# Kernel tuning notes

Hardware: AMD Instinct MI355X
Metric: run time of the kernel (lower is better)

The kernel has to match this reference:

```python
import jax, jax.numpy as jnp
import numpy as np

N_NODES = 50000
NEG_SLOPE = 0.2


def _gat_conv(x, edge_index, W, att_src, att_dst, bias, heads, out_ch, concat):
    """PyG-style GATConv (add_self_loops=True, negative_slope=0.2).
    x: [N, F_in], edge_index: [2, E] (row=src, row=dst), W: [F_in, heads*out_ch],
    att_src/att_dst: [heads, out_ch], bias: [heads*out_ch] or [out_ch]."""
    N = x.shape[0]
    # add self-loops
    loops = jnp.arange(N, dtype=edge_index.dtype)
    src = jnp.concatenate([edge_index[0], loops])
    dst = jnp.concatenate([edge_index[1], loops])

    h = (x @ W).reshape(N, heads, out_ch)                 # [N, H, C]
    a_src = jnp.einsum('nhc,hc->nh', h, att_src)          # [N, H]
    a_dst = jnp.einsum('nhc,hc->nh', h, att_dst)          # [N, H]

    e = a_src[src] + a_dst[dst]                           # [E', H]
    e = jnp.where(e >= 0, e, NEG_SLOPE * e)               # leaky_relu

    # segment softmax over incoming edges of each dst node
    e_max = jax.ops.segment_max(e, dst, num_segments=N)   # [N, H]
    e_max = jnp.where(jnp.isfinite(e_max), e_max, 0.0)
    ex = jnp.exp(e - e_max[dst])                          # [E', H]
    denom = jax.ops.segment_sum(ex, dst, num_segments=N)  # [N, H]
    alpha = ex / (denom[dst] + 1e-16)                     # [E', H]

    msg = alpha[:, :, None] * h[src]                      # [E', H, C]
    out = jax.ops.segment_sum(msg, dst, num_segments=N)   # [N, H, C]

    if concat:
        out = out.reshape(N, heads * out_ch)
    else:
        out = out.mean(axis=1)
    return out + bias


def setup_inputs() -> dict:
    key = jax.random.key(0)
    ks = jax.random.split(key, 12)
    F_in, hid, H1, C, H2 = 512, 8, 8, 40, 1
    x = jax.random.normal(ks[0], (N_NODES, F_in), dtype=jnp.float32)
    edge_index = jax.random.randint(ks[1], (2, 1600000), 0, N_NODES, dtype=jnp.int64)
    s1 = 1.0 / np.sqrt(F_in)
    s2 = 1.0 / np.sqrt(hid * H1)
    return {
        'x': x,
        'edge_index': edge_index,
        'W1': jax.random.normal(ks[2], (F_in, H1 * hid), dtype=jnp.float32) * s1,
        'att_src1': jax.random.normal(ks[3], (H1, hid), dtype=jnp.float32) * s2,
        'att_dst1': jax.random.normal(ks[4], (H1, hid), dtype=jnp.float32) * s2,
        'b1': jnp.zeros((H1 * hid,), dtype=jnp.float32),
        'W2': jax.random.normal(ks[5], (H1 * hid, H2 * C), dtype=jnp.float32) * s2,
        'att_src2': jax.random.normal(ks[6], (H2, C), dtype=jnp.float32) * 0.15,
        'att_dst2': jax.random.normal(ks[7], (H2, C), dtype=jnp.float32) * 0.15,
        'b2': jnp.zeros((C,), dtype=jnp.float32),
    }


def reference(x, edge_index, W1, att_src1, att_dst1, b1, W2, att_src2, att_dst2, b2):
    # eval mode: dropout is identity
    h = _gat_conv(x, edge_index, W1, att_src1, att_dst1, b1, heads=8, out_ch=8, concat=True)
    h = jax.nn.relu(h)
    h = _gat_conv(h, edge_index, W2, att_src2, att_dst2, b2, heads=1, out_ch=40, concat=False)
    return jax.nn.log_softmax(h, axis=1)
```

## Files before the change

kernel.cpp:

```cpp
#include <hip/hip_runtime.h>
#include <math.h>

#define NNODES 50000
#define NEG_SLOPE 0.2f
#define NB 391
#define BW 128
#define CHUNK 4096
#define CAP 8128

typedef __bf16 bf16x8 __attribute__((ext_vector_type(8)));
typedef float f32x4 __attribute__((ext_vector_type(4)));

__device__ inline float rlane(float v, int l) {
    return __uint_as_float(__builtin_amdgcn_readlane((int)__float_as_uint(v), l));
}

__global__ void prep(const float* __restrict__ W1, __bf16* __restrict__ W1b,
                     int* __restrict__ bcur) {
    int i = blockIdx.x * 256 + threadIdx.x;
    if (i < NB) bcur[i] = i * CAP;
    else if (i == NB) bcur[NB] = 0;
    if (i >= 512 * 64) return;
    int k = i >> 6, n = i & 63;
    W1b[((size_t)(k >> 3) * 64 + n) * 8 + (k & 7)] = (__bf16)W1[i];
}

__global__ __launch_bounds__(256) void bin_scatter(const int* __restrict__ ei,
                                                   int E, int N, int* bcur,
                                                   int* __restrict__ tmp) {
    __shared__ int lcnt[NB];
    __shared__ int lbase[NB];
    int tid = threadIdx.x;
    int base0 = blockIdx.x * CHUNK;
    int lim = min(base0 + CHUNK, E + N);
    for (int i = tid; i < NB; i += 256) lcnt[i] = 0;
    __syncthreads();
    for (int e = base0 + tid; e < lim; e += 256) {
        int d = (e < E) ? ei[E + e] : e - E;
        atomicAdd(&lcnt[d >> 7], 1);
    }
    __syncthreads();
    for (int b = tid; b < NB; b += 256) {
        int c = lcnt[b];
        lbase[b] = c ? atomicAdd(&bcur[b], c) : 0;
    }
    __syncthreads();
    for (int i = tid; i < NB; i += 256) lcnt[i] = 0;
    __syncthreads();
    for (int e = base0 + tid; e < lim; e += 256) {
        int s, d;
        if (e < E) { s = ei[e]; d = ei[E + e]; }
        else       { s = d = e - E; }
        int b = d >> 7;
        int p = atomicAdd(&lcnt[b], 1);
        tmp[lbase[b] + p] = ((d & 127) << 16) | s;
    }
}

__global__ __launch_bounds__(256) void csr_finalize(int* __restrict__ bcur,
                                                    const int* __restrict__ tmp,
                                                    int N, int* __restrict__ off,
                                                    int* __restrict__ off_end,
                                                    int* __restrict__ slot) {
    __shared__ int cnt[BW];
    __shared__ int cur[BW];
    __shared__ int cbase_s;
    int b = blockIdx.x, tid = threadIdx.x;
    int base = b * CAP;
    int m = bcur[b] - base;
    if (tid < BW) cnt[tid] = 0;
    __syncthreads();
    for (int i = tid; i < m; i += 256)
        atomicAdd(&cnt[(tmp[base + i] >> 16) & 127], 1);
    __syncthreads();
    if (tid == 0) cbase_s = atomicAdd(&bcur[NB], m);
    int myv = (tid < BW) ? cnt[tid] : 0;
    for (int o = 1; o < BW; o <<= 1) {
        int u = 0;
        if (tid >= o && tid < BW) u = cnt[tid - o];
        __syncthreads();
        if (tid < BW) cnt[tid] += u;
        __syncthreads();
    }
    if (tid < BW) {
        int ex = cbase_s + cnt[tid] - myv;
        cur[tid] = ex;
        int g = b * BW + tid;
        if (g < N) { off[g] = ex; off_end[g] = ex + myv; }
    }
    __syncthreads();
    for (int i = tid; i < m; i += 256) {
        int v = tmp[base + i];
        int k = (v >> 16) & 127;
        int p = atomicAdd(&cur[k], 1);
        slot[p] = v & 0xFFFF;
    }
}

__global__ __launch_bounds__(256) void gemm1_mfma(const float* __restrict__ X,
                                                  const __bf16* __restrict__ W1b,
                                                  const float* __restrict__ att_s1,
                                                  const float* __restrict__ att_d1,
                                                  __bf16* __restrict__ H1b,
                                                  float* __restrict__ a_s1,
                                                  float* __restrict__ a_d1,
                                                  int M) {
    __shared__ __bf16 As[2048];
    __shared__ __bf16 Bs[2048];
    int tid = threadIdx.x, wid = tid >> 6, lane = tid & 63;
    int quad = lane >> 4, l15 = lane & 15;
    int m0 = blockIdx.x * 64;
    f32x4 acc[4] = {{0.f, 0.f, 0.f, 0.f}, {0.f, 0.f, 0.f, 0.f},
                    {0.f, 0.f, 0.f, 0.f}, {0.f, 0.f, 0.f, 0.f}};
    int mrow = tid >> 2;
    int kq_w = tid & 3;
    int xrow = min(m0 + mrow, M - 1);
    const float* xp = X + (size_t)xrow * 512 + kq_w * 8;
    for (int kb = 0; kb < 16; ++kb) {
        float4 xa = *(const float4*)(xp + kb * 32);
        float4 xb = *(const float4*)(xp + kb * 32 + 4);
        bf16x8 av;
        av[0] = (__bf16)xa.x; av[1] = (__bf16)xa.y;
        av[2] = (__bf16)xa.z; av[3] = (__bf16)xa.w;
        av[4] = (__bf16)xb.x; av[5] = (__bf16)xb.y;
        av[6] = (__bf16)xb.z; av[7] = (__bf16)xb.w;
        *(bf16x8*)(As + ((size_t)kq_w * 64 + mrow) * 8) = av;
        *(bf16x8*)(Bs + ((size_t)wid * 64 + lane) * 8) =
            *(const bf16x8*)(W1b + ((size_t)(kb * 4 + wid) * 64 + lane) * 8);
        __syncthreads();
        bf16x8 af = *(const bf16x8*)(As + ((size_t)quad * 64 + 16 * wid + l15) * 8);
#pragma unroll
        for (int t = 0; t < 4; ++t) {
            bf16x8 bf = *(const bf16x8*)(Bs + ((size_t)quad * 64 + 16 * t + l15) * 8);
            acc[t] = __builtin_amdgcn_mfma_f32_16x16x32_bf16(af, bf, acc[t], 0, 0, 0);
        }
        __syncthreads();
    }
    float asv[4], adv[4];
#pragma unroll
    for (int t = 0; t < 4; ++t) {
        asv[t] = att_s1[16 * t + l15];
        adv[t] = att_d1[16 * t + l15];
    }
#pragma unroll
    for (int t = 0; t < 4; ++t) {
#pragma unroll
        for (int r = 0; r < 4; ++r) {
            int gm = m0 + 16 * wid + quad * 4 + r;
            if (gm < M) H1b[(size_t)gm * 64 + 16 * t + l15] = (__bf16)acc[t][r];
            float ps = acc[t][r] * asv[t];
            float pd = acc[t][r] * adv[t];
            ps += __shfl_xor(ps, 1); ps += __shfl_xor(ps, 2); ps += __shfl_xor(ps, 4);
            pd += __shfl_xor(pd, 1); pd += __shfl_xor(pd, 2); pd += __shfl_xor(pd, 4);
            if (gm < M && (l15 & 7) == 0) {
                int hh = 2 * t + (l15 >> 3);
                a_s1[(size_t)gm * 8 + hh] = ps;
                a_d1[(size_t)gm * 8 + hh] = pd;
            }
        }
    }
}

#define EDGE_GROUP1(IDX, SVAR, WVAR, HVAR, EVAR)                        \
    int SVAR = __shfl(sv, ((IDX) < deg) ? (IDX) : dm1);                 \
    float EVAR = a_src[(size_t)SVAR * 8 + eh] + adst_c;                 \
    EVAR = (EVAR >= 0.f) ? EVAR : NEG_SLOPE * EVAR;                     \
    float WVAR = ((IDX) < deg) ? __expf(EVAR) : 0.f;                    \
    bf16x8 HVAR = *(const bf16x8*)(hbase + (size_t)SVAR * 64);

__global__ __launch_bounds__(256, 8) void agg1_fused(const int* __restrict__ off,
                                                  const int* __restrict__ off_end,
                                                  const int* __restrict__ slot,
                                                  const __bf16* __restrict__ H1b,
                                                  const float* __restrict__ a_src,
                                                  const float* __restrict__ a_dst,
                                                  const float* __restrict__ b1,
                                                  const float* __restrict__ W2,
                                                  const float* __restrict__ att_src2,
                                                  const float* __restrict__ att_dst2,
                                                  __bf16* __restrict__ H2b,
                                                  float* __restrict__ a_s2,
                                                  float* __restrict__ a_d2) {
    __shared__ float W2s[64 * 40];
    int tid = threadIdx.x;
    int wid = tid >> 6, lane = tid & 63;
    for (int i = tid; i < 64 * 40; i += 256) W2s[i] = W2[i];
    int d = blockIdx.x * 4 + wid;
    int beg = off[d], end = off_end[d];
    int deg = end - beg, dm1 = deg - 1;
    int es = lane >> 3;
    int eh = lane & 7;
    float adst_c = a_dst[(size_t)d * 8 + eh];
    const __bf16* hbase = H1b + eh * 8;
    int sv = slot[beg + ((lane < deg) ? lane : dm1)];
    float acc[8] = {0.f, 0.f, 0.f, 0.f, 0.f, 0.f, 0.f, 0.f};
    float den_l = 0.f;
    {
        EDGE_GROUP1(es,      s0, w0, h0, e0)
        EDGE_GROUP1(8 + es,  s1, w1, h1, e1)
        EDGE_GROUP1(16 + es, s2, w2, h2, e2)
        EDGE_GROUP1(24 + es, s3, w3, h3, e3)
        den_l = ((w0 + w1) + (w2 + w3));
#pragma unroll
        for (int q = 0; q < 8; ++q)
            acc[q] = w0 * (float)h0[q] + w1 * (float)h1[q] +
                     w2 * (float)h2[q] + w3 * (float)h3[q];
    }
    int dcap = (deg < 64) ? deg : 64;
    for (int b = 32; b < dcap; b += 16) {
        EDGE_GROUP1(b + es,     s0, w0, h0, e0)
        EDGE_GROUP1(b + 8 + es, s1, w1, h1, e1)
        den_l += w0 + w1;
#pragma unroll
        for (int q = 0; q < 8; ++q)
            acc[q] += w0 * (float)h0[q] + w1 * (float)h1[q];
    }
    for (int i = beg + 64; i < end; i += 8) {
        int j = i + es;
        int jj = (j < end) ? j : (end - 1);
        int s = slot[jj];
        float e = a_src[(size_t)s * 8 + eh] + adst_c;
        e = (e >= 0.f) ? e : NEG_SLOPE * e;
        float w = (j < end) ? __expf(e) : 0.f;
        den_l += w;
        bf16x8 hv = *(const bf16x8*)(hbase + (size_t)s * 64);
#pragma unroll
        for (int q = 0; q < 8; ++q) acc[q] += w * (float)hv[q];
    }
#pragma unroll
    for (int m = 8; m <= 32; m <<= 1) {
        den_l += __shfl_xor(den_l, m);
#pragma unroll
        for (int q = 0; q < 8; ++q) acc[q] += __shfl_xor(acc[q], m);
    }
    float rden = 1.f / (den_l + 1e-16f);
    float vr[8];
#pragma unroll
    for (int q = 0; q < 8; ++q) {
        float t = acc[q] * rden + b1[eh * 8 + q];
        vr[q] = (t > 0.f) ? t : 0.f;
    }
    __syncthreads();
    int c = lane, cc = (c < 40) ? c : 0;
    float acc2a = 0.f, acc2b = 0.f;
#pragma unroll
    for (int k = 0; k < 64; k += 2) {
        float r0 = rlane(vr[k & 7], k >> 3);
        float r1 = rlane(vr[(k + 1) & 7], (k + 1) >> 3);
        acc2a += r0 * W2s[k * 40 + cc];
        acc2b += r1 * W2s[(k + 1) * 40 + cc];
    }
    float acc2 = acc2a + acc2b;
    H2b[(size_t)d * 64 + c] = (__bf16)((c < 40) ? acc2 : 0.f);
    float ps = (c < 40) ? acc2 * att_src2[cc] : 0.f;
    float pd = (c < 40) ? acc2 * att_dst2[cc] : 0.f;
#pragma unroll
    for (int mm = 32; mm >= 1; mm >>= 1) {
        ps += __shfl_xor(ps, mm);
        pd += __shfl_xor(pd, mm);
    }
    if (lane == 0) { a_s2[d] = ps; a_d2[d] = pd; }
}

#define EDGE_GROUP2(IDX, SVAR, WVAR, HVAR, EVAR)                        \
    int SVAR = __shfl(sv, ((IDX) < deg) ? (IDX) : dm1);                 \
    float EVAR = a_src2[SVAR] + adst;                                   \
    EVAR = (EVAR >= 0.f) ? EVAR : NEG_SLOPE * EVAR;                     \
    float WVAR = ((IDX) < deg) ? __expf(EVAR) : 0.f;                    \
    bf16x8 HVAR = *(const bf16x8*)(hbase + (size_t)SVAR * 64);

__global__ __launch_bounds__(256, 8) void agg2(const int* __restrict__ off,
                                            const int* __restrict__ off_end,
                                            const int* __restrict__ slot,
                                            const __bf16* __restrict__ H2b,
                                            const float* __restrict__ a_src2,
                                            const float* __restrict__ a_d2,
                                            const float* __restrict__ b2,
                                            float* __restrict__ out) {
    int tid = threadIdx.x;
    int wid = tid >> 6, lane = tid & 63;
    int d = blockIdx.x * 4 + wid;
    int beg = off[d], end = off_end[d];
    int deg = end - beg, dm1 = deg - 1;
    int es = lane >> 3;
    int sl = lane & 7;
    float adst = a_d2[d];
    const __bf16* hbase = H2b + sl * 8;
    bool valid = (sl < 5);
    int sv = slot[beg + ((lane < deg) ? lane : dm1)];
    float acc[8] = {0.f, 0.f, 0.f, 0.f, 0.f, 0.f, 0.f, 0.f};
    float den_l = 0.f;
    {
        EDGE_GROUP2(es,      s0, w0, h0, e0)
        EDGE_GROUP2(8 + es,  s1, w1, h1, e1)
        EDGE_GROUP2(16 + es, s2, w2, h2, e2)
        EDGE_GROUP2(24 + es, s3, w3, h3, e3)
        den_l = ((w0 + w1) + (w2 + w3));
#pragma unroll
        for (int q = 0; q < 8; ++q)
            acc[q] = w0 * (float)h0[q] + w1 * (float)h1[q] +
                     w2 * (float)h2[q] + w3 * (float)h3[q];
    }
    int dcap = (deg < 64) ? deg : 64;
    for (int b = 32; b < dcap; b += 16) {
        EDGE_GROUP2(b + es,     s0, w0, h0, e0)
        EDGE_GROUP2(b + 8 + es, s1, w1, h1, e1)
        den_l += w0 + w1;
#pragma unroll
        for (int q = 0; q < 8; ++q)
            acc[q] += w0 * (float)h0[q] + w1 * (float)h1[q];
    }
    for (int i = beg + 64; i < end; i += 8) {
        int j = i + es;
        int jj = (j < end) ? j : (end - 1);
        int s = slot[jj];
        float e = a_src2[s] + adst;
        e = (e >= 0.f) ? e : NEG_SLOPE * e;
        float w = (j < end) ? __expf(e) : 0.f;
        den_l += w;
        bf16x8 hv = *(const bf16x8*)(hbase + (size_t)s * 64);
#pragma unroll
        for (int q = 0; q < 8; ++q) acc[q] += w * (float)hv[q];
    }
#pragma unroll
    for (int m = 8; m <= 32; m <<= 1) {
        den_l += __shfl_xor(den_l, m);
#pragma unroll
        for (int q = 0; q < 8; ++q) acc[q] += __shfl_xor(acc[q], m);
    }
    float rden = 1.f / (den_l + 1e-16f);
    float v[8];
    float vm = -3.0e38f;
#pragma unroll
    for (int q = 0; q < 8; ++q) {
        v[q] = acc[q] * rden + b2[valid ? sl * 8 + q : 0];
        vm = fmaxf(vm, v[q]);
    }
    if (!valid) vm = -3.0e38f;
#pragma unroll
    for (int m = 1; m <= 4; m <<= 1) vm = fmaxf(vm, __shfl_xor(vm, m));
    float se = 0.f;
#pragma unroll
    for (int q = 0; q < 8; ++q) se += __expf(v[q] - vm);
    if (!valid) se = 0.f;
#pragma unroll
    for (int m = 1; m <= 4; m <<= 1) se += __shfl_xor(se, m);
    float lse = vm + __logf(se);
    if (es == 0 && valid) {
        f32x4 o0 = {v[0] - lse, v[1] - lse, v[2] - lse, v[3] - lse};
        f32x4 o1 = {v[4] - lse, v[5] - lse, v[6] - lse, v[7] - lse};
        *(f32x4*)(out + (size_t)d * 40 + sl * 8) = o0;
        *(f32x4*)(out + (size_t)d * 40 + sl * 8 + 4) = o1;
    }
}

extern "C" void kernel_launch(void* const* d_in, const int* in_sizes, int n_in,
                              void* d_out, int out_size, void* d_ws, size_t ws_size,
                              hipStream_t stream) {
    const float* x   = (const float*)d_in[0];
    const int*   ei  = (const int*)d_in[1];
    const float* W1  = (const float*)d_in[2];
    const float* as1 = (const float*)d_in[3];
    const float* ad1 = (const float*)d_in[4];
    const float* b1  = (const float*)d_in[5];
    const float* W2  = (const float*)d_in[6];
    const float* as2 = (const float*)d_in[7];
    const float* ad2 = (const float*)d_in[8];
    const float* b2  = (const float*)d_in[9];
    float* out = (float*)d_out;

    const int N = NNODES;
    const int E = in_sizes[1] / 2;
    const int total = E + N;

    char* ws = (char*)d_ws;
    size_t o = 0;
    auto alloc = [&](size_t bytes) -> void* {
        void* p = ws + o;
        o = (o + bytes + 255) & ~(size_t)255;
        return p;
    };
    int* bcur    = (int*)alloc((size_t)(NB + 1) * 4);
    int* off     = (int*)alloc((size_t)N * 4);
    int* off_end = (int*)alloc((size_t)N * 4);
    int* slot    = (int*)alloc((size_t)total * 4);
    int* tmp     = (int*)alloc((size_t)NB * CAP * 4);
    __bf16* W1b = (__bf16*)alloc((size_t)512 * 64 * 2);
    __bf16* H1b = (__bf16*)alloc((size_t)N * 64 * 2);
    float* a_s1 = (float*)alloc((size_t)N * 8 * 4);
    float* a_d1 = (float*)alloc((size_t)N * 8 * 4);
    __bf16* H2b = (__bf16*)alloc((size_t)N * 64 * 2);
    float* a_s2 = (float*)alloc((size_t)N * 4);
    float* a_d2 = (float*)alloc((size_t)N * 4);
    (void)ws_size; (void)n_in; (void)out_size;

    prep<<<(512 * 64 + 255) / 256, 256, 0, stream>>>(W1, W1b, bcur);
    bin_scatter<<<(total + CHUNK - 1) / CHUNK, 256, 0, stream>>>(ei, E, N, bcur, tmp);
    csr_finalize<<<NB, 256, 0, stream>>>(bcur, tmp, N, off, off_end, slot);

    gemm1_mfma<<<(N + 63) / 64, 256, 0, stream>>>(x, W1b, as1, ad1, H1b, a_s1, a_d1, N);

    agg1_fused<<<N / 4, 256, 0, stream>>>(off, off_end, slot, H1b, a_s1, a_d1, b1,
                                          W2, as2, ad2, H2b, a_s2, a_d2);

    agg2<<<N / 4, 256, 0, stream>>>(off, off_end, slot, H2b, a_s2, a_d2, b2, out);
}
```

Measured before the change: 343.5 us.

## Pack layer-2 source attention into H2 row padding and widen aggregation unroll

Stores the layer-2 source attention scalar in the unused padding of each bf16 H2 row, so agg2 obtains it from the same 16-byte gather as the features instead of a separate random load. agg1 drops the LDS staging of W2 and its block barrier and reads W2 directly from global/cache. Both aggregation loops now take four edge groups per iteration instead of two, and slot reads and output writes use nontemporal hints. The cost is a cross-lane shuffle per edge group and more register pressure from the wider unroll. Uncached W2 reads may also add latency.

```diff
diff --git a/kernel.cpp b/kernel.cpp
--- a/kernel.cpp
+++ b/kernel.cpp
@@ -10,6 +10,7 @@
 
 typedef __bf16 bf16x8 __attribute__((ext_vector_type(8)));
 typedef float f32x4 __attribute__((ext_vector_type(4)));
+typedef int i32x4 __attribute__((ext_vector_type(4)));
 
 __device__ inline float rlane(float v, int l) {
     return __uint_as_float(__builtin_amdgcn_readlane((int)__float_as_uint(v), l));
@@ -179,12 +180,9 @@
                                                   const float* __restrict__ att_src2,
                                                   const float* __restrict__ att_dst2,
                                                   __bf16* __restrict__ H2b,
-                                                  float* __restrict__ a_s2,
                                                   float* __restrict__ a_d2) {
-    __shared__ float W2s[64 * 40];
     int tid = threadIdx.x;
     int wid = tid >> 6, lane = tid & 63;
-    for (int i = tid; i < 64 * 40; i += 256) W2s[i] = W2[i];
     int d = blockIdx.x * 4 + wid;
     int beg = off[d], end = off_end[d];
     int deg = end - beg, dm1 = deg - 1;
@@ -192,7 +190,7 @@
     int eh = lane & 7;
     float adst_c = a_dst[(size_t)d * 8 + eh];
     const __bf16* hbase = H1b + eh * 8;
-    int sv = slot[beg + ((lane < deg) ? lane : dm1)];
+    int sv = __builtin_nontemporal_load(slot + beg + ((lane < deg) ? lane : dm1));
     float acc[8] = {0.f, 0.f, 0.f, 0.f, 0.f, 0.f, 0.f, 0.f};
     float den_l = 0.f;
     {
@@ -207,13 +205,16 @@
                      w2 * (float)h2[q] + w3 * (float)h3[q];
     }
     int dcap = (deg < 64) ? deg : 64;
-    for (int b = 32; b < dcap; b += 16) {
-        EDGE_GROUP1(b + es,     s0, w0, h0, e0)
-        EDGE_GROUP1(b + 8 + es, s1, w1, h1, e1)
-        den_l += w0 + w1;
+    for (int b = 32; b < dcap; b += 32) {
+        EDGE_GROUP1(b + es,      s0, w0, h0, e0)
+        EDGE_GROUP1(b + 8 + es,  s1, w1, h1, e1)
+        EDGE_GROUP1(b + 16 + es, s2, w2, h2, e2)
+        EDGE_GROUP1(b + 24 + es, s3, w3, h3, e3)
+        den_l += ((w0 + w1) + (w2 + w3));
 #pragma unroll
         for (int q = 0; q < 8; ++q)
-            acc[q] += w0 * (float)h0[q] + w1 * (float)h1[q];
+            acc[q] += w0 * (float)h0[q] + w1 * (float)h1[q] +
+                      w2 * (float)h2[q] + w3 * (float)h3[q];
     }
     for (int i = beg + 64; i < end; i += 8) {
         int j = i + es;
@@ -240,18 +241,18 @@
         float t = acc[q] * rden + b1[eh * 8 + q];
         vr[q] = (t > 0.f) ? t : 0.f;
     }
-    __syncthreads();
     int c = lane, cc = (c < 40) ? c : 0;
+    const float* wp = W2 + cc;
     float acc2a = 0.f, acc2b = 0.f;
 #pragma unroll
     for (int k = 0; k < 64; k += 2) {
         float r0 = rlane(vr[k & 7], k >> 3);
         float r1 = rlane(vr[(k + 1) & 7], (k + 1) >> 3);
-        acc2a += r0 * W2s[k * 40 + cc];
-        acc2b += r1 * W2s[(k + 1) * 40 + cc];
+        acc2a += r0 * wp[k * 40];
+        acc2b += r1 * wp[(k + 1) * 40];
     }
     float acc2 = acc2a + acc2b;
-    H2b[(size_t)d * 64 + c] = (__bf16)((c < 40) ? acc2 : 0.f);
+    if (c < 40) H2b[(size_t)d * 64 + c] = (__bf16)acc2;
     float ps = (c < 40) ? acc2 * att_src2[cc] : 0.f;
     float pd = (c < 40) ? acc2 * att_dst2[cc] : 0.f;
 #pragma unroll
@@ -259,21 +260,24 @@
         ps += __shfl_xor(ps, mm);
         pd += __shfl_xor(pd, mm);
     }
-    if (lane == 0) { a_s2[d] = ps; a_d2[d] = pd; }
-}
-
-#define EDGE_GROUP2(IDX, SVAR, WVAR, HVAR, EVAR)                        \
+    if (lane == 0) {
+        a_d2[d] = pd;
+        *(float*)(H2b + (size_t)d * 64 + 40) = ps;
+    }
+}
+
+#define EDGE_GROUP2(IDX, SVAR, WVAR, HVAR)                              \
     int SVAR = __shfl(sv, ((IDX) < deg) ? (IDX) : dm1);                 \
-    float EVAR = a_src2[SVAR] + adst;                                   \
-    EVAR = (EVAR >= 0.f) ? EVAR : NEG_SLOPE * EVAR;                     \
-    float WVAR = ((IDX) < deg) ? __expf(EVAR) : 0.f;                    \
-    bf16x8 HVAR = *(const bf16x8*)(hbase + (size_t)SVAR * 64);
+    i32x4 rv_##HVAR = *(const i32x4*)(hbase + (size_t)SVAR * 64);       \
+    bf16x8 HVAR = __builtin_bit_cast(bf16x8, rv_##HVAR);                \
+    float e_##HVAR = __uint_as_float(__shfl(rv_##HVAR[0], asl)) + adst; \
+    e_##HVAR = (e_##HVAR >= 0.f) ? e_##HVAR : NEG_SLOPE * e_##HVAR;     \
+    float WVAR = ((IDX) < deg) ? __expf(e_##HVAR) : 0.f;
 
 __global__ __launch_bounds__(256, 8) void agg2(const int* __restrict__ off,
                                             const int* __restrict__ off_end,
                                             const int* __restrict__ slot,
                                             const __bf16* __restrict__ H2b,
-                                            const float* __restrict__ a_src2,
                                             const float* __restrict__ a_d2,
                                             const float* __restrict__ b2,
                                             float* __restrict__ out) {
@@ -284,17 +288,18 @@
     int deg = end - beg, dm1 = deg - 1;
     int es = lane >> 3;
     int sl = lane & 7;
+    int asl = (lane & 56) | 5;
     float adst = a_d2[d];
     const __bf16* hbase = H2b + sl * 8;
     bool valid = (sl < 5);
-    int sv = slot[beg + ((lane < deg) ? lane : dm1)];
+    int sv = __builtin_nontemporal_load(slot + beg + ((lane < deg) ? lane : dm1));
     float acc[8] = {0.f, 0.f, 0.f, 0.f, 0.f, 0.f, 0.f, 0.f};
     float den_l = 0.f;
     {
-        EDGE_GROUP2(es,      s0, w0, h0, e0)
-        EDGE_GROUP2(8 + es,  s1, w1, h1, e1)
-        EDGE_GROUP2(16 + es, s2, w2, h2, e2)
-        EDGE_GROUP2(24 + es, s3, w3, h3, e3)
+        EDGE_GROUP2(es,      s0, w0, h0)
+        EDGE_GROUP2(8 + es,  s1, w1, h1)
+        EDGE_GROUP2(16 + es, s2, w2, h2)
+        EDGE_GROUP2(24 + es, s3, w3, h3)
         den_l = ((w0 + w1) + (w2 + w3));
 #pragma unroll
         for (int q = 0; q < 8; ++q)
@@ -302,23 +307,27 @@
                      w2 * (float)h2[q] + w3 * (float)h3[q];
     }
     int dcap = (deg < 64) ? deg : 64;
-    for (int b = 32; b < dcap; b += 16) {
-        EDGE_GROUP2(b + es,     s0, w0, h0, e0)
-        EDGE_GROUP2(b + 8 + es, s1, w1, h1, e1)
-        den_l += w0 + w1;
+    for (int b = 32; b < dcap; b += 32) {
+        EDGE_GROUP2(b + es,      s0, w0, h0)
+        EDGE_GROUP2(b + 8 + es,  s1, w1, h1)
+        EDGE_GROUP2(b + 16 + es, s2, w2, h2)
+        EDGE_GROUP2(b + 24 + es, s3, w3, h3)
+        den_l += ((w0 + w1) + (w2 + w3));
 #pragma unroll
         for (int q = 0; q < 8; ++q)
-            acc[q] += w0 * (float)h0[q] + w1 * (float)h1[q];
+            acc[q] += w0 * (float)h0[q] + w1 * (float)h1[q] +
+                      w2 * (float)h2[q] + w3 * (float)h3[q];
     }
     for (int i = beg + 64; i < end; i += 8) {
         int j = i + es;
         int jj = (j < end) ? j : (end - 1);
         int s = slot[jj];
-        float e = a_src2[s] + adst;
+        i32x4 rv = *(const i32x4*)(hbase + (size_t)s * 64);
+        bf16x8 hv = __builtin_bit_cast(bf16x8, rv);
+        float e = __uint_as_float(__shfl(rv[0], asl)) + adst;
         e = (e >= 0.f) ? e : NEG_SLOPE * e;
         float w = (j < end) ? __expf(e) : 0.f;
         den_l += w;
-        bf16x8 hv = *(const bf16x8*)(hbase + (size_t)s * 64);
 #pragma unroll
         for (int q = 0; q < 8; ++q) acc[q] += w * (float)hv[q];
     }
@@ -349,8 +358,8 @@
     if (es == 0 && valid) {
         f32x4 o0 = {v[0] - lse, v[1] - lse, v[2] - lse, v[3] - lse};
         f32x4 o1 = {v[4] - lse, v[5] - lse, v[6] - lse, v[7] - lse};
-        *(f32x4*)(out + (size_t)d * 40 + sl * 8) = o0;
-        *(f32x4*)(out + (size_t)d * 40 + sl * 8 + 4) = o1;
+        __builtin_nontemporal_store(o0, (f32x4*)(out + (size_t)d * 40 + sl * 8));
+        __builtin_nontemporal_store(o1, (f32x4*)(out + (size_t)d * 40 + sl * 8 + 4));
     }
 }
 
@@ -390,7 +399,6 @@
     float* a_s1 = (float*)alloc((size_t)N * 8 * 4);
     float* a_d1 = (float*)alloc((size_t)N * 8 * 4);
     __bf16* H2b = (__bf16*)alloc((size_t)N * 64 * 2);
-    float* a_s2 = (float*)alloc((size_t)N * 4);
     float* a_d2 = (float*)alloc((size_t)N * 4);
     (void)ws_size; (void)n_in; (void)out_size;
 
@@ -401,7 +409,7 @@
     gemm1_mfma<<<(N + 63) / 64, 256, 0, stream>>>(x, W1b, as1, ad1, H1b, a_s1, a_d1, N);
 
     agg1_fused<<<N / 4, 256, 0, stream>>>(off, off_end, slot, H1b, a_s1, a_d1, b1,
-                                          W2, as2, ad2, H2b, a_s2, a_d2);
-
-    agg2<<<N / 4, 256, 0, stream>>>(off, off_end, slot, H2b, a_s2, a_d2, b2, out);
-}
+                                          W2, as2, ad2, H2b, a_d2);
+
+    agg2<<<N / 4, 256, 0, stream>>>(off, off_end, slot, H2b, a_d2, b2, out);
+}
```

Result: slower. 420.6 us (+22.4%).
